# Kernel tuning notes

Measured on AMD Instinct MI355X. Metric: run time of the kernel, lower is better.

Reference implementation:

```python
import jax, jax.numpy as jnp
import numpy as np
import math

EPS = 1e-5
N_HEADS = 4


def _ln(x, g, b):
    mu = jnp.mean(x, axis=-1, keepdims=True)
    var = jnp.mean((x - mu) ** 2, axis=-1, keepdims=True)
    return (x - mu) * jax.lax.rsqrt(var + EPS) * g + b


def _eq_ln(s, v, g, b, vscale):
    # scalar LayerNorm + equivariant vector norm rescaling
    s = _ln(s, g, b)
    vn = jnp.sqrt(jnp.sum(v * v, axis=-1, keepdims=True))  # (B,N,C,1)
    v = v / (vn + EPS) * jnp.mean(vn, axis=-2, keepdims=True) * vscale[None, None, :, None]
    return s, v


def _block(s, v, pos, Wq, bq, Wk, bk, Wv, bv, Wo, bo, w_dist, b_dist, Wvv, Wvo,
           g1, be1, vs1, g2, be2, vs2, Wf1, bf1, Wf2, bf2, Wfv1, Wfv2):
    B, N, S = s.shape
    D = S // N_HEADS
    # --- norm1 + attention ---
    sn, vn = _eq_ln(s, v, g1, be1, vs1)
    q = (sn @ Wq + bq).reshape(B, N, N_HEADS, D)
    k = (sn @ Wk + bk).reshape(B, N, N_HEADS, D)
    vs = (sn @ Wv + bv).reshape(B, N, N_HEADS, D)
    attn = jnp.einsum('bnhd,bmhd->bhnm', q, k) / math.sqrt(D)
    # pairwise Euclidean distance via the |x|^2 + |y|^2 - 2xy trick (clamped for sqrt safety)
    p2 = jnp.sum(pos * pos, axis=-1)  # (B,N)
    d2 = p2[:, :, None] + p2[:, None, :] - 2.0 * jnp.einsum('bnd,bmd->bnm', pos, pos)
    dist = jnp.sqrt(jnp.maximum(d2, 1e-12))  # (B,N,N)
    # dist_proj: Linear(1 -> n_heads) + Softplus, applied per pair
    bias = jax.nn.softplus(dist[..., None] * w_dist + b_dist)  # (B,N,N,H)
    attn = jax.nn.softmax(attn - jnp.transpose(bias, (0, 3, 1, 2)), axis=-1)  # (B,H,N,N)
    attn_mean = jnp.mean(attn, axis=1)  # (B,N,N)
    s_attn = jnp.einsum('bhnm,bmhd->bnhd', attn, vs).reshape(B, N, S) @ Wo + bo
    # vector channel mixing + rotation by head-averaged attention
    v_mix = jnp.einsum('bncx,ce->bnex', vn, Wvv)          # (B,N,C,3)
    v_attn = jnp.einsum('bnm,bmcx->bncx', attn_mean, v_mix)
    v_attn = jnp.einsum('bncx,ce->bnex', v_attn, Wvo)
    s = s + s_attn
    v = v + v_attn
    # --- norm2 + FFN ---
    sn, vn = _eq_ln(s, v, g2, be2, vs2)
    s = s + (jax.nn.gelu(sn @ Wf1 + bf1, approximate=False) @ Wf2 + bf2)
    v = v + jnp.einsum('bnhx,hc->bncx', jnp.einsum('bncx,ch->bnhx', vn, Wfv1), Wfv2)
    return s, v


def setup_inputs() -> dict:
    B, N, S, C, H = 4, 2048, 256, 64, N_HEADS
    key = jax.random.key(0)
    ks = jax.random.split(key, 24)

    def nrm(k, shape, scale=0.02):
        return jax.random.normal(k, shape, dtype=jnp.float32) * scale

    return {
        's': jax.random.normal(ks[0], (B, N, S), dtype=jnp.float32),
        'v': jax.random.normal(ks[1], (B, N, C, 3), dtype=jnp.float32),
        'pos': jax.random.normal(ks[2], (B, N, 3), dtype=jnp.float32),
        'Wq': nrm(ks[3], (S, S)), 'bq': nrm(ks[4], (S,)),
        'Wk': nrm(ks[5], (S, S)), 'bk': nrm(ks[6], (S,)),
        'Wv': nrm(ks[7], (S, S)), 'bv': nrm(ks[8], (S,)),
        'Wo': nrm(ks[9], (S, S)), 'bo': nrm(ks[10], (S,)),
        'w_dist': nrm(ks[11], (H,), 0.5), 'b_dist': nrm(ks[12], (H,), 0.5),
        'Wvv': nrm(ks[13], (C, C)), 'Wvo': nrm(ks[14], (C, C)),
        'g1': jnp.ones((S,), jnp.float32), 'be1': jnp.zeros((S,), jnp.float32),
        'vs1': jnp.ones((C,), jnp.float32),
        'g2': jnp.ones((S,), jnp.float32), 'be2': jnp.zeros((S,), jnp.float32),
        'vs2': jnp.ones((C,), jnp.float32),
        'Wf1': nrm(ks[15], (S, 4 * S)), 'bf1': nrm(ks[16], (4 * S,)),
        'Wf2': nrm(ks[17], (4 * S, S)), 'bf2': nrm(ks[18], (S,)),
        'Wfv1': nrm(ks[19], (C, 4 * C)), 'Wfv2': nrm(ks[20], (4 * C, C)),
    }


def reference(s, v, pos, Wq, bq, Wk, bk, Wv, bv, Wo, bo, w_dist, b_dist, Wvv, Wvo,
              g1, be1, vs1, g2, be2, vs2, Wf1, bf1, Wf2, bf2, Wfv1, Wfv2):
    return _block(s, v, pos, Wq, bq, Wk, bk, Wv, bv, Wo, bo, w_dist, b_dist, Wvv, Wvo,
                  g1, be1, vs1, g2, be2, vs2, Wf1, bf1, Wf2, bf2, Wfv1, Wfv2)
```

## Files before the change

### kernel.cpp

```cpp
#include <hip/hip_runtime.h>
#include <hip/hip_bf16.h>

using bf16 = __hip_bfloat16;
typedef __attribute__((ext_vector_type(8))) short short8;
typedef __attribute__((ext_vector_type(4))) float float4v;
typedef __attribute__((ext_vector_type(16))) float f32x16;
typedef __attribute__((ext_vector_type(4))) unsigned uint4v;

__device__ __forceinline__ float b2f(bf16 x){ return __bfloat162float(x); }
__device__ __forceinline__ bf16  f2b(float x){ return __float2bfloat16(x); }
__device__ __forceinline__ bf16  tob(float x){ return f2b(x); }
__device__ __forceinline__ bf16  tob(bf16 x){ return x; }
__device__ __forceinline__ float frcp(float x){ return __builtin_amdgcn_rcpf(x); }
__device__ __forceinline__ float bs2f(short s){
  unsigned u = ((unsigned)(unsigned short)s) << 16;
  return __builtin_bit_cast(float, u);
}
__device__ __forceinline__ unsigned cvt_pk_bf16(float lo, float hi){
  unsigned r; asm("v_cvt_pk_bf16_f32 %0, %1, %2" : "=v"(r) : "v"(lo), "v"(hi)); return r;
}
__device__ __forceinline__ void plswap(unsigned &a, unsigned &b){
  asm("v_permlane32_swap_b32 %0, %1" : "+v"(a), "+v"(b));
}

#define EPSV 1e-5f
#define Z16 {0.f,0.f,0.f,0.f,0.f,0.f,0.f,0.f,0.f,0.f,0.f,0.f,0.f,0.f,0.f,0.f}

__global__ __launch_bounds__(256) void pos_kernel(const float* __restrict__ pos,
                                                  float* __restrict__ posf, int rows){
  int r = blockIdx.x*256 + threadIdx.x;
  if (r >= rows) return;
  float x = pos[3*r], y = pos[3*r+1], z = pos[3*r+2];
  posf[4*r] = x; posf[4*r+1] = y; posf[4*r+2] = z; posf[4*r+3] = x*x + y*y + z*z;
}

struct WTDesc { const float* src; bf16* dst; int rows, cols; };
struct WTPack { WTDesc d[10]; };

__global__ __launch_bounds__(256) void wtrans_kernel(WTPack p){
  WTDesc w = p.d[blockIdx.z];
  long r0 = (long)blockIdx.y*32, c0 = (long)blockIdx.x*32;
  if (r0 >= w.rows || c0 >= w.cols) return;
  __shared__ bf16 tile[32][33];
  int tx = threadIdx.x & 31, ty = threadIdx.x >> 5;
#pragma unroll
  for (int i = ty; i < 32; i += 8) tile[i][tx] = f2b(w.src[(r0+i)*w.cols + c0 + tx]);
  __syncthreads();
#pragma unroll
  for (int i = ty; i < 32; i += 8) w.dst[(c0+i)*w.rows + r0 + tx] = tile[tx][i];
}

template<typename TI>
__global__ __launch_bounds__(256) void transpose_kernel(
    const TI* __restrict__ in, long ldin, long is1, long is2,
    bf16* __restrict__ out, long ldout, long os1, long os2, int Z2)
{
  int z = blockIdx.z, z1 = z / Z2, z2 = z - z1*Z2;
  in  += (long)z1*is1 + (long)z2*is2;
  out += (long)z1*os1 + (long)z2*os2;
  __shared__ bf16 tile[32][33];
  int tx = threadIdx.x & 31, ty = threadIdx.x >> 5;
  long r0 = (long)blockIdx.y*32, c0 = (long)blockIdx.x*32;
#pragma unroll
  for (int i = ty; i < 32; i += 8) tile[i][tx] = tob(in[(r0+i)*ldin + c0 + tx]);
  __syncthreads();
#pragma unroll
  for (int i = ty; i < 32; i += 8) out[(c0+i)*ldout + r0 + tx] = tile[tx][i];
}

__global__ __launch_bounds__(256) void bcat_kernel(const float* __restrict__ bq,
                                                   const float* __restrict__ bk,
                                                   const float* __restrict__ bv,
                                                   float* __restrict__ bqkv){
  int j = blockIdx.x*256 + threadIdx.x;
  if (j >= 768) return;
  bqkv[j] = (j < 256) ? bq[j] : (j < 512) ? bk[j-256] : bv[j-512];
}

__global__ __launch_bounds__(256) void ln_kernel(const float* __restrict__ x,
                                                 const float* __restrict__ g,
                                                 const float* __restrict__ be,
                                                 bf16* __restrict__ out){
  const long row = blockIdx.x;
  const int t = threadIdx.x;
  __shared__ float r1[256], r2[256];
  float v = x[(row<<8) + t];
  r1[t] = v; r2[t] = v*v; __syncthreads();
  for (int s=128;s>0;s>>=1){
    if (t<s){ r1[t] += r1[t+s]; r2[t] += r2[t+s]; }
    __syncthreads();
  }
  const float mu = r1[0] * (1.f/256.f);
  const float var = r2[0] * (1.f/256.f) - mu*mu;
  const float rstd = rsqrtf(fmaxf(var, 0.f) + EPSV);
  out[(row<<8)+t] = f2b((v-mu)*rstd*g[t] + be[t]);
}

__global__ __launch_bounds__(192) void vnorm1_kernel(const float* __restrict__ vin,
                                                     const float* __restrict__ vs1,
                                                     bf16* __restrict__ vnX){
  const long row = blockIdx.x;
  const int t = threadIdx.x;
  __shared__ float vv[192], nrm[64];
  __shared__ float smean;
  vv[t] = vin[row*192 + t];
  __syncthreads();
  if (t < 64){
    float a = vv[3*t], b = vv[3*t+1], c = vv[3*t+2];
    nrm[t] = sqrtf(a*a + b*b + c*c);
  }
  __syncthreads();
  if (t == 0){ float s = 0.f; for (int i=0;i<64;i++) s += nrm[i]; smean = s*(1.f/64.f); }
  __syncthreads();
  const int c = t/3, x = t - 3*c;
  const float val = vv[t] / (nrm[c] + EPSV) * smean * vs1[c];
  vnX[row*192 + x*64 + c] = f2b(val);
}

__global__ __launch_bounds__(192) void vnorm2_kernel(const float* __restrict__ v2X,
                                                     const float* __restrict__ vs2,
                                                     bf16* __restrict__ vn2X){
  const long row = blockIdx.x;
  const int t = threadIdx.x;
  __shared__ float vv[192], nrm[64];
  __shared__ float smean;
  vv[t] = v2X[row*192 + t];
  __syncthreads();
  if (t < 64){
    float a = vv[t], b = vv[t+64], c = vv[t+128];
    nrm[t] = sqrtf(a*a + b*b + c*c);
  }
  __syncthreads();
  if (t == 0){ float s = 0.f; for (int i=0;i<64;i++) s += nrm[i]; smean = s*(1.f/64.f); }
  __syncthreads();
  const int c = t & 63;
  vn2X[row*192 + t] = f2b(vv[t] / (nrm[c] + EPSV) * smean * vs2[c]);
}

__global__ __launch_bounds__(256) void knorm_kernel(const bf16* __restrict__ qkv,
                                                    float* __restrict__ kmax){
  const int bh = blockIdx.x, b = bh>>2, h = bh&3;
  const int t = threadIdx.x;
  __shared__ float red[256];
  float mx = 0.f;
  for (int r=0;r<8;r++){
    long row = (long)b*2048 + r*256 + t;
    const short8* kp = (const short8*)(qkv + row*768 + 256 + h*64);
    float ss = 0.f;
#pragma unroll
    for (int c=0;c<8;c++){
      short8 v = kp[c];
#pragma unroll
      for (int j=0;j<8;j++){ float f = bs2f(v[j]); ss = fmaf(f,f,ss); }
    }
    mx = fmaxf(mx, ss);
  }
  red[t] = mx; __syncthreads();
  for (int s=128;s>0;s>>=1){ if (t<s) red[t] = fmaxf(red[t], red[t+s]); __syncthreads(); }
  if (t==0) kmax[bh] = sqrtf(red[0]);
}

#define ATT_K_OFF   0
#define ATT_V_OFF   4096
#define ATT_X_OFF   9216
#define ATT_P_OFF   24576
#define ATT_TILE    25088
#define ATT_GRP     50176
#define ATT_LACC    98304
#define ATT_SMEM    100352

__global__ __launch_bounds__(512, 2) void attn_kernel(
    const bf16* __restrict__ qkv,
    const bf16* __restrict__ vsT,
    const bf16* __restrict__ vmixT,
    const float* __restrict__ posf,
    const float* __restrict__ kmaxA,
    const float* __restrict__ w_dist, const float* __restrict__ b_dist,
    bf16* __restrict__ sA,
    bf16* __restrict__ slab)
{
  __shared__ __align__(16) char smem[ATT_SMEM];
  const int qb = blockIdx.x;
  const int bh = blockIdx.y;
  const int b  = bh >> 2, h = bh & 3;
  const int tid = threadIdx.x;
  const int w = tid >> 6, lane = tid & 63;
  const int g = w >> 2, qw = w & 3;
  const int lq = lane & 31, hi = lane >> 5;
  const int gtid = tid & 255;

  const int qloc = qb*128 + qw*32 + lq;
  const long rowQ = (long)b*2048 + qloc;

  short8 qf[4];
  {
    const bf16* qp = qkv + rowQ*768 + h*64 + hi*8;
#pragma unroll
    for (int kc=0;kc<4;kc++) qf[kc] = *(const short8*)(qp + kc*16);
  }
  float q2 = 0.f;
#pragma unroll
  for (int kc=0;kc<4;kc++)
#pragma unroll
    for (int j=0;j<8;j++){ float qv = bs2f(qf[kc][j]); q2 = fmaf(qv,qv,q2); }
  q2 += __shfl_xor(q2, 32);
  const float mxs = sqrtf(q2) * kmaxA[bh] * 0.125f;
  const float wh = w_dist[h], bhd = b_dist[h];
  const float4v pn = *(const float4v*)(posf + (long)b*8192 + (long)qloc*4);

  f32x16 O[2]  = {Z16, Z16};
  f32x16 VM[6] = {Z16, Z16, Z16, Z16, Z16, Z16};
  float lacc = 0.f;

  short8 stK, stV, stX0, stX1, stX2; float4v stP;
  const int sm = gtid >> 3, sc = gtid & 7;
  const int vd = gtid >> 2, vc = gtid & 3;
  const bf16* Kg = qkv + (long)b*2048*768 + 256 + h*64;
  const bf16* Vg = vsT + (long)b*524288 + (long)h*131072;
  const bf16* Xg = vmixT + (long)b*393216;
  const float* Pg = posf + (long)b*8192;
  char* gbase = smem + g*ATT_GRP;

  auto LOADT = [&](int m0){
    stK  = *(const short8*)(Kg + (long)(m0+sm)*768 + sc*8);
    stV  = *(const short8*)(Vg + (long)vd*2048 + m0 + vc*8);
    stX0 = *(const short8*)(Xg + (long)vd*2048 + m0 + vc*8);
    stX1 = *(const short8*)(Xg + (long)(64+vd)*2048 + m0 + vc*8);
    stX2 = *(const short8*)(Xg + (long)(128+vd)*2048 + m0 + vc*8);
    if (gtid < 32) stP = *(const float4v*)(Pg + (long)(m0+gtid)*4);
  };
  auto WRITET = [&](char* buf){
    *(short8*)(buf + ATT_K_OFF + sm*128 + ((sc ^ (sm&7))<<4)) = stK;
    *(short8*)(buf + ATT_V_OFF + vd*80 + vc*16) = stV;
    *(short8*)(buf + ATT_X_OFF + vd*80 + vc*16) = stX0;
    *(short8*)(buf + ATT_X_OFF + (64+vd)*80 + vc*16) = stX1;
    *(short8*)(buf + ATT_X_OFF + (128+vd)*80 + vc*16) = stX2;
    if (gtid < 32) *(float4v*)(buf + ATT_P_OFF + gtid*16) = stP;
  };

  auto COMPUTE = [&](const char* buf){
    const char* Kb = buf + ATT_K_OFF;
    const char* Vb = buf + ATT_V_OFF;
    const char* Xb = buf + ATT_X_OFF;
    const float4v* pmb = (const float4v*)(buf + ATT_P_OFF);
    f32x16 S = Z16;
#pragma unroll
    for (int kc=0;kc<4;kc++){
      short8 kf = *(const short8*)(Kb + lq*128 + (((kc*2+hi) ^ (lq&7))<<4));
      S = __builtin_amdgcn_mfma_f32_32x32x16_bf16(kf, qf[kc], S, 0, 0, 0);
    }
    float P[16];
#pragma unroll
    for (int gg=0; gg<4; gg++){
#pragma unroll
      for (int i=0;i<4;i++){
        float4v pm = pmb[gg*8 + hi*4 + i];
        float d2 = pn[3] + pm[3] - 2.f*(pn[0]*pm[0] + pn[1]*pm[1] + pn[2]*pm[2]);
        float dist = sqrtf(fmaxf(d2, 1e-12f));
        float sig = frcp(1.f + __expf(fmaf(dist, wh, bhd)));
        float p = __expf(fmaf(S[gg*4+i], 0.125f, -mxs)) * sig;
        lacc += p;
        P[gg*4+i] = p;
      }
    }
    unsigned pk[8];
#pragma unroll
    for (int t=0;t<8;t++) pk[t] = cvt_pk_bf16(P[2*t], P[2*t+1]);
    plswap(pk[0], pk[2]); plswap(pk[1], pk[3]);
    plswap(pk[4], pk[6]); plswap(pk[5], pk[7]);
    uint4v y0v = {pk[0], pk[1], pk[2], pk[3]};
    uint4v y1v = {pk[4], pk[5], pk[6], pk[7]};
    short8 Y0 = __builtin_bit_cast(short8, y0v);
    short8 Y1 = __builtin_bit_cast(short8, y1v);
#pragma unroll
    for (int dblk=0; dblk<2; dblk++){
      short8 v0 = *(const short8*)(Vb + (dblk*32+lq)*80 + hi*16);
      short8 v1 = *(const short8*)(Vb + (dblk*32+lq)*80 + 32 + hi*16);
      O[dblk] = __builtin_amdgcn_mfma_f32_32x32x16_bf16(v0, Y0, O[dblk], 0,0,0);
      O[dblk] = __builtin_amdgcn_mfma_f32_32x32x16_bf16(v1, Y1, O[dblk], 0,0,0);
    }
#pragma unroll
    for (int eblk=0; eblk<6; eblk++){
      short8 x0 = *(const short8*)(Xb + (eblk*32+lq)*80 + hi*16);
      short8 x1 = *(const short8*)(Xb + (eblk*32+lq)*80 + 32 + hi*16);
      VM[eblk] = __builtin_amdgcn_mfma_f32_32x32x16_bf16(x0, Y0, VM[eblk], 0,0,0);
      VM[eblk] = __builtin_amdgcn_mfma_f32_32x32x16_bf16(x1, Y1, VM[eblk], 0,0,0);
    }
  };

  LOADT(g*32);
  WRITET(gbase);
  __syncthreads();
#pragma unroll 1
  for (int i=0; i<32; ++i){
    if (i < 31) LOADT((2*(i+1)+g)*32);
    COMPUTE(gbase + (i&1)*ATT_TILE);
    if (i < 31) WRITET(gbase + ((i+1)&1)*ATT_TILE);
    __syncthreads();
  }

  float* laccT = (float*)(smem + ATT_LACC);
  laccT[w*64 + lane] = lacc;
  if (g == 1){
    float* Od = (float*)(smem + (qw*64+lane)*128);
#pragma unroll
    for (int r=0;r<16;r++){ Od[r] = O[0][r]; Od[16+r] = O[1][r]; }
  }
  __syncthreads();
  const float lsum = laccT[qw*64+lq] + laccT[qw*64+32+lq]
                   + laccT[(4+qw)*64+lq] + laccT[(4+qw)*64+32+lq];
  if (g == 0){
    const float* Od = (const float*)(smem + (qw*64+lane)*128);
#pragma unroll
    for (int r=0;r<16;r++){ O[0][r] += Od[r]; O[1][r] += Od[16+r]; }
  }
  __syncthreads();
  if (g == 0){
    float* Vd = (float*)(smem + (qw*64+lane)*384);
#pragma unroll
    for (int e=0;e<6;e++)
#pragma unroll
      for (int r=0;r<16;r++) Vd[e*16+r] = VM[e][r];
  }
  __syncthreads();
  if (g == 1){
    const float* Vd = (const float*)(smem + (qw*64+lane)*384);
#pragma unroll
    for (int e=0;e<6;e++)
#pragma unroll
      for (int r=0;r<16;r++) VM[e][r] += Vd[e*16+r];
  }
  __syncthreads();

  const float sinv = frcp(lsum);
  if (g == 0){
    char* scr = smem + qw*12544;
#pragma unroll
    for (int dblk=0; dblk<2; dblk++)
#pragma unroll
      for (int pp=0; pp<8; pp++){
        const int r = 2*pp;
        const int d = dblk*32 + (r&3) + 8*(r>>2) + 4*hi;
        unsigned u = cvt_pk_bf16(O[dblk][r]*sinv, O[dblk][r+1]*sinv);
        *(unsigned*)(scr + lq*136 + d*2) = u;
      }
  } else {
    const float vinv = 0.25f * sinv;
    char* scr = smem + ATT_GRP + qw*12544;
#pragma unroll
    for (int eblk=0; eblk<6; eblk++)
#pragma unroll
      for (int pp=0; pp<8; pp++){
        const int r = 2*pp;
        const int e = eblk*32 + (r&3) + 8*(r>>2) + 4*hi;
        unsigned u = cvt_pk_bf16(VM[eblk][r]*vinv, VM[eblk][r+1]*vinv);
        *(unsigned*)(scr + lq*392 + e*2) = u;
      }
  }
  __syncthreads();
  if (g == 0){
    const char* scr = smem + qw*12544;
    const int q = lane >> 1, half = lane & 1;
    const char* src = scr + q*136 + half*64;
    char* dst = (char*)(sA + (long)(b*2048 + qb*128 + qw*32 + q)*256 + h*64 + half*32);
#pragma unroll
    for (int i=0;i<8;i++)
      *(unsigned long long*)(dst + i*8) = *(const unsigned long long*)(src + i*8);
  } else {
    const char* scr = smem + ATT_GRP + qw*12544;
    const int q = lane >> 1, half = lane & 1;
    const char* src = scr + q*392 + half*192;
    char* dst = (char*)(slab + (long)h*1572864
                        + (long)(b*2048 + qb*128 + qw*32 + q)*192 + half*96);
#pragma unroll
    for (int i=0;i<24;i++)
      *(unsigned long long*)(dst + i*8) = *(const unsigned long long*)(src + i*8);
  }
}

__global__ __launch_bounds__(256) void hred_kernel(const bf16* __restrict__ slab,
                                                   bf16* __restrict__ out){
  long i = (long)blockIdx.x*256 + threadIdx.x;
  if (i >= 196608) return;
  const short8* s0 = (const short8*)slab + i;
  short8 a = s0[0], b = s0[196608], c = s0[2*196608], d = s0[3*196608];
  short8 o;
#pragma unroll
  for (int j=0;j<8;j++){
    float f = bs2f(a[j]) + bs2f(b[j]) + bs2f(c[j]) + bs2f(d[j]);
    bf16 hv = f2b(f); o[j] = *(short*)&hv;
  }
  ((short8*)out)[i] = o;
}

template<int MT, int NT, int ACT, int OUTM, int RXIL, int CXIL>
__global__ __launch_bounds__(64) void gemm_kernel(
    const bf16* __restrict__ A, long lda, long As1, long As2,
    const bf16* __restrict__ BT, long ldb, long Bs1, long Bs2,
    const float* __restrict__ bias,
    const float* __restrict__ resid, long ldr, long Rs1, long Rs2,
    void* __restrict__ Cv, long ldc, long Cs1, long Cs2,
    int K, int Z2, int KS)
{
  int z = blockIdx.z;
  int zz = z / KS, ks = z - zz*KS;
  int z1 = zz / Z2, z2 = zz - z1*Z2;
  A  += (long)z1*As1 + (long)z2*As2 + (long)ks*K;
  BT += (long)z1*Bs1 + (long)z2*Bs2 + (long)ks*K;
  if (resid) resid += (long)z1*Rs1 + (long)z2*Rs2;
  const long cbase = (long)z1*Cs1 + (long)z2*Cs2;

  const int lane = threadIdx.x;
  const int col = lane & 15, quad = lane >> 4;
  const long rowA0 = (long)blockIdx.y*(16*MT);
  const long colB0 = (long)blockIdx.x*(16*NT);

  float4v acc[MT][NT];
#pragma unroll
  for (int m=0;m<MT;m++)
#pragma unroll
    for (int n=0;n<NT;n++) acc[m][n] = (float4v){0.f,0.f,0.f,0.f};

  const bf16* ap[MT];
  const bf16* bp[NT];
#pragma unroll
  for (int m=0;m<MT;m++) ap[m] = A + (rowA0 + m*16 + col)*lda + quad*8;
#pragma unroll
  for (int n=0;n<NT;n++) bp[n] = BT + (colB0 + n*16 + col)*ldb + quad*8;

  for (int k0 = 0; k0 < K; k0 += 32){
    short8 a[MT], bb[NT];
#pragma unroll
    for (int m=0;m<MT;m++){ a[m] = *(const short8*)ap[m]; ap[m] += 32; }
#pragma unroll
    for (int n=0;n<NT;n++){ bb[n] = *(const short8*)bp[n]; bp[n] += 32; }
#pragma unroll
    for (int m=0;m<MT;m++)
#pragma unroll
      for (int n=0;n<NT;n++)
        acc[m][n] = __builtin_amdgcn_mfma_f32_16x16x32_bf16(a[m], bb[n], acc[m][n], 0, 0, 0);
  }

#pragma unroll
  for (int m=0;m<MT;m++){
    const long ri = rowA0 + m*16 + quad*4;
#pragma unroll
    for (int n=0;n<NT;n++){
      const long cj = colB0 + n*16 + col;
      const float bbias = bias ? bias[cj] : 0.f;
#pragma unroll
      for (int r=0;r<4;r++){
        const long ci = ri + r;
        float val = acc[m][n][r] + bbias;
        if (ACT == 1) val = 0.5f*val*(1.f + erff(val*0.70710678118654752f));
        if (resid){
          const long raddr = RXIL ? ((ci/3)*192 + cj*3 + (ci%3)) : (ci*ldr + cj);
          val += resid[raddr];
        }
        const long caddr = CXIL ? (cbase + (ci/3)*192 + cj*3 + (ci%3))
                                : (cbase + ci*ldc + cj);
        if (OUTM == 0)      ((bf16*)Cv)[caddr] = f2b(val);
        else if (OUTM == 1) ((float*)Cv)[caddr] = val;
        else                unsafeAtomicAdd(&((float*)Cv)[caddr], val);
      }
    }
  }
}

extern "C" void kernel_launch(void* const* d_in, const int* in_sizes, int n_in,
                              void* d_out, int out_size, void* d_ws, size_t ws_size,
                              hipStream_t stream)
{
  const float* s    = (const float*)d_in[0];
  const float* v    = (const float*)d_in[1];
  const float* pos  = (const float*)d_in[2];
  const float* Wq   = (const float*)d_in[3];
  const float* bq   = (const float*)d_in[4];
  const float* Wk   = (const float*)d_in[5];
  const float* bk   = (const float*)d_in[6];
  const float* Wv   = (const float*)d_in[7];
  const float* bv   = (const float*)d_in[8];
  const float* Wo   = (const float*)d_in[9];
  const float* bo   = (const float*)d_in[10];
  const float* w_d  = (const float*)d_in[11];
  const float* b_d  = (const float*)d_in[12];
  const float* Wvv  = (const float*)d_in[13];
  const float* Wvo  = (const float*)d_in[14];
  const float* g1   = (const float*)d_in[15];
  const float* be1  = (const float*)d_in[16];
  const float* vs1  = (const float*)d_in[17];
  const float* g2   = (const float*)d_in[18];
  const float* be2  = (const float*)d_in[19];
  const float* vs2  = (const float*)d_in[20];
  const float* Wf1  = (const float*)d_in[21];
  const float* bf1  = (const float*)d_in[22];
  const float* Wf2  = (const float*)d_in[23];
  const float* bf2  = (const float*)d_in[24];
  const float* Wfv1 = (const float*)d_in[25];
  const float* Wfv2 = (const float*)d_in[26];

  float* outS = (float*)d_out;
  float* outV = outS + (size_t)4*2048*256;

  char* w = (char*)d_ws;
  size_t o = 0;
  auto alloc = [&](size_t bytes)->char* {
    char* p = w + o;
    o = (o + bytes + 255) & ~(size_t)255;
    return p;
  };
  float* posf  = (float*)alloc(131072);
  bf16* WqkvT = (bf16*)alloc(393216);
  bf16* WoT   = (bf16*)alloc(131072);
  bf16* Wf1T  = (bf16*)alloc(524288);
  bf16* Wf2T  = (bf16*)alloc(524288);
  bf16* WvvT  = (bf16*)alloc(8192);
  bf16* WvoT  = (bf16*)alloc(8192);
  bf16* Wfv1T = (bf16*)alloc(32768);
  bf16* Wfv2T = (bf16*)alloc(32768);
  float* bqkv = (float*)alloc(3072);
  float* kmax = (float*)alloc(64);
  bf16* sn    = (bf16*)alloc(4194304);
  bf16* qkv   = (bf16*)alloc(12582912);
  bf16* vsT   = (bf16*)alloc(4194304);
  bf16* sA    = (bf16*)alloc(4194304);
  float* s2   = (float*)alloc(8388608);
  bf16* vnX   = (bf16*)alloc(3145728);
  bf16* vmixX = (bf16*)alloc(3145728);
  bf16* vmixXT= (bf16*)alloc(3145728);
  float* v2X  = (float*)alloc(6291456);
  bf16* slab  = (bf16*)alloc(12582912);
  bf16* h1    = (bf16*)alloc(16777216);
  bf16* vn2X  = vnX;
  bf16* tvXb  = vmixX;
  bf16* hv    = qkv;
  if (o > ws_size) return;

  pos_kernel<<<32, 256, 0, stream>>>(pos, posf, 8192);
  WTPack pk;
  pk.d[0] = {Wq,   WqkvT,          256, 256};
  pk.d[1] = {Wk,   WqkvT + 65536,  256, 256};
  pk.d[2] = {Wv,   WqkvT + 131072, 256, 256};
  pk.d[3] = {Wo,   WoT,            256, 256};
  pk.d[4] = {Wf1,  Wf1T,           256, 1024};
  pk.d[5] = {Wf2,  Wf2T,           1024, 256};
  pk.d[6] = {Wvv,  WvvT,           64, 64};
  pk.d[7] = {Wvo,  WvoT,           64, 64};
  pk.d[8] = {Wfv1, Wfv1T,          64, 256};
  pk.d[9] = {Wfv2, Wfv2T,          256, 64};
  wtrans_kernel<<<dim3(32,32,10), 256, 0, stream>>>(pk);
  bcat_kernel<<<3, 256, 0, stream>>>(bq, bk, bv, bqkv);

  ln_kernel<<<8192, 256, 0, stream>>>(s, g1, be1, sn);
  vnorm1_kernel<<<8192, 192, 0, stream>>>(v, vs1, vnX);

  gemm_kernel<2,4,0,0,0,0><<<dim3(1,768,1), 64, 0, stream>>>(vnX,64,0,0, WvvT,64,0,0,
      nullptr, nullptr,0,0,0, vmixX,64,0,0, 64, 1, 1);
  transpose_kernel<bf16><<<dim3(6,64,4), 256, 0, stream>>>(vmixX, 192, 393216,0,
      vmixXT, 2048, 393216,0, 1);

  gemm_kernel<2,4,0,0,0,0><<<dim3(12,256,1), 64, 0, stream>>>(sn,256,0,0, WqkvT,256,0,0,
      bqkv, nullptr,0,0,0, qkv,768,0,0, 256, 1, 1);
  transpose_kernel<bf16><<<dim3(2,64,16), 256, 0, stream>>>(qkv+512, 768, 1572864,64,
      vsT, 2048, 524288,131072, 4);

  knorm_kernel<<<16, 256, 0, stream>>>(qkv, kmax);
  attn_kernel<<<dim3(16,16), 512, 0, stream>>>(qkv, vsT, vmixXT, posf, kmax,
      w_d, b_d, sA, slab);
  hred_kernel<<<768, 256, 0, stream>>>(slab, tvXb);

  gemm_kernel<2,4,0,1,0,0><<<dim3(4,256,1), 64, 0, stream>>>(sA,256,0,0, WoT,256,0,0,
      bo, s,256,0,0, s2,256,0,0, 256, 1, 1);

  gemm_kernel<2,4,0,1,1,0><<<dim3(1,768,1), 64, 0, stream>>>(tvXb,64,0,0, WvoT,64,0,0,
      nullptr, v,0,0,0, v2X,64,0,0, 64, 1, 1);

  ln_kernel<<<8192, 256, 0, stream>>>(s2, g2, be2, sn);
  gemm_kernel<2,4,1,0,0,0><<<dim3(16,256,1), 64, 0, stream>>>(sn,256,0,0, Wf1T,256,0,0,
      bf1, nullptr,0,0,0, h1,1024,0,0, 256, 1, 1);
  gemm_kernel<2,4,0,1,0,0><<<dim3(4,256,1), 64, 0, stream>>>(h1,1024,0,0, Wf2T,1024,0,0,
      bf2, s2,256,0,0, outS,256,0,0, 1024, 1, 1);

  vnorm2_kernel<<<8192, 192, 0, stream>>>(v2X, vs2, vn2X);
  gemm_kernel<2,4,0,0,0,0><<<dim3(4,768,1), 64, 0, stream>>>(vn2X,64,0,0, Wfv1T,64,0,0,
      nullptr, nullptr,0,0,0, hv,256,0,0, 64, 1, 1);
  gemm_kernel<2,4,0,1,0,1><<<dim3(1,768,1), 64, 0, stream>>>(hv,256,0,0, Wfv2T,256,0,0,
      nullptr, v2X,64,0,0, outV,0,0,0, 256, 1, 1);
}
```

Baseline: 427.5 us.

## Swizzle GEMM blocks across XCDs, pad attention reduction scratch, fold distance FMAs

Adds an optional block-index remap to the GEMM kernel that hands each XCD a contiguous band of row tiles, so blocks that share A rows sit on the same L2. It is turned on for the QKV, Wo, FFN and vector-FFN GEMMs. The attention epilogue's cross-group reduction now uses odd-stride (33/49 float) padded LDS rows and splits the 6-tile VM exchange into two halves, to cut bank conflicts and LDS footprint at the cost of two extra barriers. The pairwise distance expression is also rewritten as a chain of FMAs with -2·pos precomputed per query.

```diff
diff --git a/kernel.cpp b/kernel.cpp
--- a/kernel.cpp
+++ b/kernel.cpp
@@ -207,6 +207,7 @@
   const float mxs = sqrtf(q2) * kmaxA[bh] * 0.125f;
   const float wh = w_dist[h], bhd = b_dist[h];
   const float4v pn = *(const float4v*)(posf + (long)b*8192 + (long)qloc*4);
+  const float m2x = -2.f*pn[0], m2y = -2.f*pn[1], m2z = -2.f*pn[2], pnw = pn[3];
 
   f32x16 O[2]  = {Z16, Z16};
   f32x16 VM[6] = {Z16, Z16, Z16, Z16, Z16, Z16};
@@ -255,7 +256,7 @@
 #pragma unroll
       for (int i=0;i<4;i++){
         float4v pm = pmb[gg*8 + hi*4 + i];
-        float d2 = pn[3] + pm[3] - 2.f*(pn[0]*pm[0] + pn[1]*pm[1] + pn[2]*pm[2]);
+        float d2 = fmaf(m2x, pm[0], fmaf(m2y, pm[1], fmaf(m2z, pm[2], pnw + pm[3])));
         float dist = sqrtf(fmaxf(d2, 1e-12f));
         float sig = frcp(1.f + __expf(fmaf(dist, wh, bhd)));
         float p = __expf(fmaf(S[gg*4+i], 0.125f, -mxs)) * sig;
@@ -302,7 +303,7 @@
   float* laccT = (float*)(smem + ATT_LACC);
   laccT[w*64 + lane] = lacc;
   if (g == 1){
-    float* Od = (float*)(smem + (qw*64+lane)*128);
+    float* Od = (float*)(smem + ATT_GRP) + (qw*64+lane)*33;
 #pragma unroll
     for (int r=0;r<16;r++){ Od[r] = O[0][r]; Od[16+r] = O[1][r]; }
   }
@@ -310,27 +311,30 @@
   const float lsum = laccT[qw*64+lq] + laccT[qw*64+32+lq]
                    + laccT[(4+qw)*64+lq] + laccT[(4+qw)*64+32+lq];
   if (g == 0){
-    const float* Od = (const float*)(smem + (qw*64+lane)*128);
+    const float* Od = (const float*)(smem + ATT_GRP) + (qw*64+lane)*33;
 #pragma unroll
     for (int r=0;r<16;r++){ O[0][r] += Od[r]; O[1][r] += Od[16+r]; }
   }
   __syncthreads();
-  if (g == 0){
-    float* Vd = (float*)(smem + (qw*64+lane)*384);
-#pragma unroll
-    for (int e=0;e<6;e++)
-#pragma unroll
-      for (int r=0;r<16;r++) Vd[e*16+r] = VM[e][r];
-  }
-  __syncthreads();
-  if (g == 1){
-    const float* Vd = (const float*)(smem + (qw*64+lane)*384);
-#pragma unroll
-    for (int e=0;e<6;e++)
-#pragma unroll
-      for (int r=0;r<16;r++) VM[e][r] += Vd[e*16+r];
-  }
-  __syncthreads();
+#pragma unroll
+  for (int hf=0; hf<2; hf++){
+    if (g == 0){
+      float* Vd = (float*)smem + (qw*64+lane)*49;
+#pragma unroll
+      for (int e=0;e<3;e++)
+#pragma unroll
+        for (int r=0;r<16;r++) Vd[e*16+r] = VM[hf*3+e][r];
+    }
+    __syncthreads();
+    if (g == 1){
+      const float* Vd = (const float*)smem + (qw*64+lane)*49;
+#pragma unroll
+      for (int e=0;e<3;e++)
+#pragma unroll
+        for (int r=0;r<16;r++) VM[hf*3+e][r] += Vd[e*16+r];
+    }
+    __syncthreads();
+  }
 
   const float sinv = frcp(lsum);
   if (g == 0){
@@ -393,7 +397,7 @@
   ((short8*)out)[i] = o;
 }
 
-template<int MT, int NT, int ACT, int OUTM, int RXIL, int CXIL>
+template<int MT, int NT, int ACT, int OUTM, int RXIL, int CXIL, int SWZ>
 __global__ __launch_bounds__(64) void gemm_kernel(
     const bf16* __restrict__ A, long lda, long As1, long As2,
     const bf16* __restrict__ BT, long ldb, long Bs1, long Bs2,
@@ -410,10 +414,21 @@
   if (resid) resid += (long)z1*Rs1 + (long)z2*Rs2;
   const long cbase = (long)z1*Cs1 + (long)z2*Cs2;
 
+  int bx = blockIdx.x, by = blockIdx.y;
+  if (SWZ){
+    const int nx = gridDim.x, ny = gridDim.y;
+    long lin = (long)by*nx + bx;
+    const int xcd = (int)(lin & 7);
+    long idx = lin >> 3;
+    const int rpx = ny >> 3;
+    by = xcd*rpx + (int)(idx / nx);
+    bx = (int)(idx % nx);
+  }
+
   const int lane = threadIdx.x;
   const int col = lane & 15, quad = lane >> 4;
-  const long rowA0 = (long)blockIdx.y*(16*MT);
-  const long colB0 = (long)blockIdx.x*(16*NT);
+  const long rowA0 = (long)by*(16*MT);
+  const long colB0 = (long)bx*(16*NT);
 
   float4v acc[MT][NT];
 #pragma unroll
@@ -554,12 +569,12 @@
   ln_kernel<<<8192, 256, 0, stream>>>(s, g1, be1, sn);
   vnorm1_kernel<<<8192, 192, 0, stream>>>(v, vs1, vnX);
 
-  gemm_kernel<2,4,0,0,0,0><<<dim3(1,768,1), 64, 0, stream>>>(vnX,64,0,0, WvvT,64,0,0,
+  gemm_kernel<2,4,0,0,0,0,0><<<dim3(1,768,1), 64, 0, stream>>>(vnX,64,0,0, WvvT,64,0,0,
       nullptr, nullptr,0,0,0, vmixX,64,0,0, 64, 1, 1);
   transpose_kernel<bf16><<<dim3(6,64,4), 256, 0, stream>>>(vmixX, 192, 393216,0,
       vmixXT, 2048, 393216,0, 1);
 
-  gemm_kernel<2,4,0,0,0,0><<<dim3(12,256,1), 64, 0, stream>>>(sn,256,0,0, WqkvT,256,0,0,
+  gemm_kernel<2,4,0,0,0,0,1><<<dim3(12,256,1), 64, 0, stream>>>(sn,256,0,0, WqkvT,256,0,0,
       bqkv, nullptr,0,0,0, qkv,768,0,0, 256, 1, 1);
   transpose_kernel<bf16><<<dim3(2,64,16), 256, 0, stream>>>(qkv+512, 768, 1572864,64,
       vsT, 2048, 524288,131072, 4);
@@ -569,21 +584,21 @@
       w_d, b_d, sA, slab);
   hred_kernel<<<768, 256, 0, stream>>>(slab, tvXb);
 
-  gemm_kernel<2,4,0,1,0,0><<<dim3(4,256,1), 64, 0, stream>>>(sA,256,0,0, WoT,256,0,0,
+  gemm_kernel<2,4,0,1,0,0,1><<<dim3(4,256,1), 64, 0, stream>>>(sA,256,0,0, WoT,256,0,0,
       bo, s,256,0,0, s2,256,0,0, 256, 1, 1);
 
-  gemm_kernel<2,4,0,1,1,0><<<dim3(1,768,1), 64, 0, stream>>>(tvXb,64,0,0, WvoT,64,0,0,
+  gemm_kernel<2,4,0,1,1,0,0><<<dim3(1,768,1), 64, 0, stream>>>(tvXb,64,0,0, WvoT,64,0,0,
       nullptr, v,0,0,0, v2X,64,0,0, 64, 1, 1);
 
   ln_kernel<<<8192, 256, 0, stream>>>(s2, g2, be2, sn);
-  gemm_kernel<2,4,1,0,0,0><<<dim3(16,256,1), 64, 0, stream>>>(sn,256,0,0, Wf1T,256,0,0,
+  gemm_kernel<2,4,1,0,0,0,1><<<dim3(16,256,1), 64, 0, stream>>>(sn,256,0,0, Wf1T,256,0,0,
       bf1, nullptr,0,0,0, h1,1024,0,0, 256, 1, 1);
-  gemm_kernel<2,4,0,1,0,0><<<dim3(4,256,1), 64, 0, stream>>>(h1,1024,0,0, Wf2T,1024,0,0,
+  gemm_kernel<2,4,0,1,0,0,1><<<dim3(4,256,1), 64, 0, stream>>>(h1,1024,0,0, Wf2T,1024,0,0,
       bf2, s2,256,0,0, outS,256,0,0, 1024, 1, 1);
 
   vnorm2_kernel<<<8192, 192, 0, stream>>>(v2X, vs2, vn2X);
-  gemm_kernel<2,4,0,0,0,0><<<dim3(4,768,1), 64, 0, stream>>>(vn2X,64,0,0, Wfv1T,64,0,0,
+  gemm_kernel<2,4,0,0,0,0,1><<<dim3(4,768,1), 64, 0, stream>>>(vn2X,64,0,0, Wfv1T,64,0,0,
       nullptr, nullptr,0,0,0, hv,256,0,0, 64, 1, 1);
-  gemm_kernel<2,4,0,1,0,1><<<dim3(1,768,1), 64, 0, stream>>>(hv,256,0,0, Wfv2T,256,0,0,
+  gemm_kernel<2,4,0,1,0,1,0><<<dim3(1,768,1), 64, 0, stream>>>(hv,256,0,0, Wfv2T,256,0,0,
       nullptr, v2X,64,0,0, outV,0,0,0, 256, 1, 1);
 }
```

Measured after the change: 425.9 us. No clear change (-0.4%).
